# Kernel optimization log

Measured on AMD Instinct MI355X. Metric: run time of the kernel, lower is better.

Reference implementation:

```python
import jax, jax.numpy as jnp
import numpy as np

B, S, DM = 4, 4096, 1024
H, DH = 16, 64          # num_attention_heads, attention_head_size
K = 128                 # Linformer projection dim (k_dims)


def setup_inputs() -> dict:
    key = jax.random.key(0)
    ks = jax.random.split(key, 9)
    s = 1.0 / np.sqrt(DM)
    return {
        "hidden_states": jax.random.normal(ks[0], (B, S, DM), jnp.float32),
        "Wq": jax.random.normal(ks[1], (DM, DM), jnp.float32) * s,
        "bq": jax.random.normal(ks[2], (DM,), jnp.float32) * 0.02,
        "Wk": jax.random.normal(ks[3], (DM, DM), jnp.float32) * s,
        "bk": jax.random.normal(ks[4], (DM,), jnp.float32) * 0.02,
        "Wv": jax.random.normal(ks[5], (DM, DM), jnp.float32) * s,
        "bv": jax.random.normal(ks[6], (DM,), jnp.float32) * 0.02,
        # E, D: [k_dims, max_input_len], init randn/sqrt(k_dims) as in torch module
        "E": jax.random.normal(ks[7], (K, S), jnp.float32) / np.sqrt(K),
        "D": jax.random.normal(ks[8], (K, S), jnp.float32) / np.sqrt(K),
    }


def reference(hidden_states, Wq, bq, Wk, bk, Wv, bv, E, D):
    b, s, _ = hidden_states.shape

    def heads(x):  # [b,s,DM] -> [b,H,s,DH]
        return x.reshape(b, s, H, DH).transpose(0, 2, 1, 3)

    # torch Linear: y = x @ W.T + b
    q = heads(hidden_states @ Wq.T + bq)   # [b,H,s,DH]
    k = heads(hidden_states @ Wk.T + bk)   # [b,H,s,DH]
    v = heads(hidden_states @ Wv.T + bv)   # [b,H,s,DH]

    # Linformer low-rank projection along the sequence axis
    pk = jnp.einsum('ks,bhsd->bhkd', E[:, :s], k)  # [b,H,K,DH]
    pv = jnp.einsum('ks,bhsd->bhkd', D[:, :s], v)  # [b,H,K,DH]

    scores = jnp.einsum('bhsd,bhkd->bhsk', q, pk) / np.sqrt(DH).astype(np.float32)
    probs = jax.nn.softmax(scores, axis=-1)        # [b,H,s,K]
    ctx = jnp.einsum('bhsk,bhkd->bhsd', probs, pv) # [b,H,s,DH]
    return ctx.transpose(0, 2, 1, 3).reshape(b, s, H * DH)
```

## Files before the change

### kernel.cpp

```cpp
#include <hip/hip_runtime.h>
#include <hip/hip_bf16.h>
#include <stdint.h>


typedef __attribute__((ext_vector_type(8))) _Float16 f16x8;
typedef __attribute__((ext_vector_type(4))) _Float16 f16x4;
typedef __attribute__((ext_vector_type(4))) float    f32x4;

__device__ __forceinline__ f32x4 mfma16(f16x8 a, f16x8 b, f32x4 c) {
    return __builtin_amdgcn_mfma_f32_16x16x32_f16(a, b, c, 0, 0, 0);
}

__device__ __forceinline__ void gload16(const void* g, void* l) {
    __builtin_amdgcn_global_load_lds(
        (const __attribute__((address_space(1))) void*)g,
        (__attribute__((address_space(3))) void*)l, 16, 0, 0);
}

__global__ __launch_bounds__(256) void cvt_f16(const float* __restrict__ in,
                                               _Float16* __restrict__ out, int n4) {
    int i = blockIdx.x * 256 + threadIdx.x;
    int stride = gridDim.x * 256;
    for (; i < n4; i += stride) {
        f32x4 v = reinterpret_cast<const f32x4*>(in)[i];
        f16x4 o;
#pragma unroll
        for (int j = 0; j < 4; ++j) o[j] = (_Float16)v[j];
        reinterpret_cast<f16x4*>(out)[i] = o;
    }
}

__global__ __launch_bounds__(256) void cvt_f16_2(const float* __restrict__ in0,
                                                 _Float16* __restrict__ out0,
                                                 const float* __restrict__ in1,
                                                 _Float16* __restrict__ out1, int n4) {
    const float* in = blockIdx.y ? in1 : in0;
    _Float16* out = blockIdx.y ? out1 : out0;
    int i = blockIdx.x * 256 + threadIdx.x;
    int stride = gridDim.x * 256;
    for (; i < n4; i += stride) {
        f32x4 v = reinterpret_cast<const f32x4*>(in)[i];
        f16x4 o;
#pragma unroll
        for (int j = 0; j < 4; ++j) o[j] = (_Float16)v[j];
        reinterpret_cast<f16x4*>(out)[i] = o;
    }
}

__global__ __launch_bounds__(256) void cvt_hilo2(const float* __restrict__ in0,
                                                 _Float16* __restrict__ hi0,
                                                 _Float16* __restrict__ lo0,
                                                 const float* __restrict__ in1,
                                                 _Float16* __restrict__ hi1,
                                                 _Float16* __restrict__ lo1, int n4) {
    const float* in = blockIdx.y ? in1 : in0;
    _Float16* hi = blockIdx.y ? hi1 : hi0;
    _Float16* lo = blockIdx.y ? lo1 : lo0;
    int i = blockIdx.x * 256 + threadIdx.x;
    int stride = gridDim.x * 256;
    for (; i < n4; i += stride) {
        f32x4 v = reinterpret_cast<const f32x4*>(in)[i];
        f16x4 h, l;
#pragma unroll
        for (int j = 0; j < 4; ++j) {
            _Float16 hb = (_Float16)v[j];
            h[j] = hb;
            l[j] = (_Float16)(v[j] - (float)hb);
        }
        reinterpret_cast<f16x4*>(hi)[i] = h;
        reinterpret_cast<f16x4*>(lo)[i] = l;
    }
}

__global__ __launch_bounds__(256) void rowsum_k(const float* __restrict__ E,
                                                const float* __restrict__ D,
                                                float* __restrict__ sE,
                                                float* __restrict__ sD) {
    __shared__ float red[256];
    const int blk = blockIdx.x;
    const float* src = (blk < 128) ? E : D;
    float* dst = (blk < 128) ? sE : sD;
    const int row = blk & 127;
    float s = 0.f;
    for (int i = threadIdx.x; i < 4096; i += 256) s += src[(size_t)row * 4096 + i];
    red[threadIdx.x] = s;
    __syncthreads();
    for (int off = 128; off > 0; off >>= 1) {
        if ((int)threadIdx.x < off) red[threadIdx.x] += red[threadIdx.x + off];
        __syncthreads();
    }
    if (threadIdx.x == 0) dst[row] = red[0];
}

__global__ __launch_bounds__(256) void gemm_q_f16(
    const _Float16* __restrict__ A, const _Float16* __restrict__ B,
    const float* __restrict__ bias, _Float16* __restrict__ Q) {
    const int Kd = 1024, N = 1024, NT = 16;
    __shared__ _Float16 Asm[2][128 * 64];
    __shared__ _Float16 Bsm[2][128 * 64];
    const int tid = threadIdx.x, lane = tid & 63, wave = tid >> 6;
    const int l15 = lane & 15, lg = lane >> 4;
    const int row0 = blockIdx.x * 128, col0 = blockIdx.y * 128;
    const int wr = (wave >> 1) * 64, wc = (wave & 1) * 64;
    f32x4 acc[4][4];
#pragma unroll
    for (int m = 0; m < 4; ++m)
#pragma unroll
        for (int n = 0; n < 4; ++n) acc[m][n] = (f32x4)0.0f;

    const _Float16* aSrc[4];
    const _Float16* bSrc[4];
    int ub[4];
#pragma unroll
    for (int it = 0; it < 4; ++it) {
        int u = it * 256 + tid;
        int r = u >> 3, c = u & 7;
        int sc = (c ^ (r & 7)) * 8;
        aSrc[it] = A + (size_t)(row0 + r) * Kd + sc;
        bSrc[it] = B + (size_t)(col0 + r) * Kd + sc;
        ub[it] = it * 256 + wave * 64;
    }
    auto stage = [&](int buf, int t) {
        const int k0 = t * 64;
#pragma unroll
        for (int it = 0; it < 4; ++it) {
            gload16(aSrc[it] + k0, &Asm[buf][ub[it] * 8]);
            gload16(bSrc[it] + k0, &Bsm[buf][ub[it] * 8]);
        }
    };

    stage(0, 0);
#pragma unroll 1
    for (int t = 0; t < NT; ++t) {
        const int cur = t & 1;
        if (t < NT - 1) {
            stage(cur ^ 1, t + 1);
            asm volatile("s_waitcnt vmcnt(8)" ::: "memory");
        } else {
            asm volatile("s_waitcnt vmcnt(0)" ::: "memory");
        }
        __builtin_amdgcn_s_barrier();
#pragma unroll
        for (int kk = 0; kk < 2; ++kk) {
            f16x8 af[4], bfr[4];
#pragma unroll
            for (int m = 0; m < 4; ++m)
                af[m] = *reinterpret_cast<const f16x8*>(
                    &Asm[cur][(wr + m * 16 + l15) * 64 + (((kk * 4 + lg) ^ (l15 & 7)) * 8)]);
#pragma unroll
            for (int n = 0; n < 4; ++n)
                bfr[n] = *reinterpret_cast<const f16x8*>(
                    &Bsm[cur][(wc + n * 16 + l15) * 64 + (((kk * 4 + lg) ^ (l15 & 7)) * 8)]);
#pragma unroll
            for (int m = 0; m < 4; ++m)
#pragma unroll
                for (int n = 0; n < 4; ++n) acc[m][n] = mfma16(af[m], bfr[n], acc[m][n]);
        }
        __builtin_amdgcn_s_barrier();
    }
#pragma unroll
    for (int m = 0; m < 4; ++m)
#pragma unroll
        for (int n = 0; n < 4; ++n) {
            int colg = col0 + wc + n * 16 + l15;
            float bi = bias[colg];
#pragma unroll
            for (int r = 0; r < 4; ++r) {
                int rowg = row0 + wr + m * 16 + lg * 4 + r;
                Q[(size_t)rowg * N + colg] = (_Float16)(acc[m][n][r] + bi);
            }
        }
}

__global__ __launch_bounds__(256) void eproj2(const _Float16* __restrict__ EB,
                                              const _Float16* __restrict__ DB,
                                              const _Float16* __restrict__ X,
                                              float* __restrict__ EHf,
                                              float* __restrict__ DHf) {
    __shared__ _Float16 Ea[128 * 72];
    __shared__ _Float16 BT[128 * 72];
    const int tid = threadIdx.x, lane = tid & 63, wave = tid >> 6;
    const int l15 = lane & 15, lg = lane >> 4;
    const int sc = blockIdx.x;
    const int n0 = blockIdx.y * 128;
    const int bb = blockIdx.z & 3;
    const _Float16* Emat = (blockIdx.z >> 2) ? DB : EB;
    float* Of = (blockIdx.z >> 2) ? DHf : EHf;
    const int wr = (wave >> 1) * 64, wc = (wave & 1) * 64;
    const int nb = tid & 31, sb = tid >> 5;
    f32x4 acc[4][4];
#pragma unroll
    for (int m = 0; m < 4; ++m)
#pragma unroll
        for (int n = 0; n < 4; ++n) acc[m][n] = (f32x4)0.0f;

    for (int ks = 0; ks < 512; ks += 64) {
        const int s0 = sc * 512 + ks;
        __syncthreads();
#pragma unroll
        for (int i = 0; i < 4; ++i) {
            int u = tid + 256 * i;
            int r = u >> 3, c8 = (u & 7) * 8;
            *reinterpret_cast<f16x8*>(&Ea[r * 72 + c8]) =
                *reinterpret_cast<const f16x8*>(Emat + (size_t)r * 4096 + s0 + c8);
        }
        {
            f16x4 rr[8];
#pragma unroll
            for (int i = 0; i < 8; ++i)
                rr[i] = *reinterpret_cast<const f16x4*>(
                    X + (size_t)(bb * 4096 + s0 + sb * 8 + i) * 1024 + n0 + nb * 4);
#pragma unroll
            for (int j = 0; j < 4; ++j) {
                f16x8 w;
#pragma unroll
                for (int i = 0; i < 8; ++i) w[i] = rr[i][j];
                *reinterpret_cast<f16x8*>(&BT[(nb * 4 + j) * 72 + sb * 8]) = w;
            }
        }
        __syncthreads();
#pragma unroll
        for (int kk = 0; kk < 2; ++kk) {
            f16x8 af[4], bfr[4];
#pragma unroll
            for (int m = 0; m < 4; ++m)
                af[m] = *reinterpret_cast<const f16x8*>(
                    &Ea[(wr + m * 16 + l15) * 72 + kk * 32 + lg * 8]);
#pragma unroll
            for (int n = 0; n < 4; ++n)
                bfr[n] = *reinterpret_cast<const f16x8*>(
                    &BT[(wc + n * 16 + l15) * 72 + kk * 32 + lg * 8]);
#pragma unroll
            for (int m = 0; m < 4; ++m)
#pragma unroll
                for (int n = 0; n < 4; ++n) acc[m][n] = mfma16(af[m], bfr[n], acc[m][n]);
        }
    }
#pragma unroll
    for (int m = 0; m < 4; ++m)
#pragma unroll
        for (int n = 0; n < 4; ++n)
#pragma unroll
            for (int r = 0; r < 4; ++r)
                atomicAdd(&Of[(size_t)(bb * 128 + wr + m * 16 + lg * 4 + r) * 1024 +
                              n0 + wc + n * 16 + l15],
                          acc[m][n][r]);
}

__global__ __launch_bounds__(256) void gemm_split2(
    const float* __restrict__ A0, const _Float16* __restrict__ Bh0,
    const _Float16* __restrict__ Bl0, const float* __restrict__ bias0,
    const float* __restrict__ rs0, _Float16* __restrict__ PKH,
    const float* __restrict__ A1, const _Float16* __restrict__ Bh1,
    const _Float16* __restrict__ Bl1, const float* __restrict__ bias1,
    const float* __restrict__ rs1, _Float16* __restrict__ PVT) {
    const int Kd = 1024;
    const float* A = blockIdx.z ? A1 : A0;
    const _Float16* Bh = blockIdx.z ? Bh1 : Bh0;
    const _Float16* Bl = blockIdx.z ? Bl1 : Bl0;
    const float* bias = blockIdx.z ? bias1 : bias0;
    const float* rowscale = blockIdx.z ? rs1 : rs0;
    __shared__ _Float16 Ah[64 * 40], Al[64 * 40], Bhs[64 * 40], Bls[64 * 40];
    const int tid = threadIdx.x, lane = tid & 63, wave = tid >> 6;
    const int l15 = lane & 15, lg = lane >> 4;
    const int row0 = blockIdx.x * 64, col0 = blockIdx.y * 64;
    const int wr = (wave >> 1) * 32, wc = (wave & 1) * 32;
    f32x4 acc[2][2];
#pragma unroll
    for (int m = 0; m < 2; ++m)
#pragma unroll
        for (int n = 0; n < 2; ++n) acc[m][n] = (f32x4)0.0f;

    const int r = tid >> 2, c8 = (tid & 3) * 8;
    for (int k0 = 0; k0 < Kd; k0 += 32) {
        __syncthreads();
        {
            const float* src = A + (size_t)(row0 + r) * Kd + k0 + c8;
            f32x4 v0 = *reinterpret_cast<const f32x4*>(src);
            f32x4 v1 = *reinterpret_cast<const f32x4*>(src + 4);
            f16x8 h8, l8;
#pragma unroll
            for (int j = 0; j < 4; ++j) {
                _Float16 hb = (_Float16)v0[j];
                h8[j] = hb; l8[j] = (_Float16)(v0[j] - (float)hb);
            }
#pragma unroll
            for (int j = 0; j < 4; ++j) {
                _Float16 hb = (_Float16)v1[j];
                h8[4 + j] = hb; l8[4 + j] = (_Float16)(v1[j] - (float)hb);
            }
            *reinterpret_cast<f16x8*>(&Ah[r * 40 + c8]) = h8;
            *reinterpret_cast<f16x8*>(&Al[r * 40 + c8]) = l8;
            *reinterpret_cast<f16x8*>(&Bhs[r * 40 + c8]) =
                *reinterpret_cast<const f16x8*>(Bh + (size_t)(col0 + r) * Kd + k0 + c8);
            *reinterpret_cast<f16x8*>(&Bls[r * 40 + c8]) =
                *reinterpret_cast<const f16x8*>(Bl + (size_t)(col0 + r) * Kd + k0 + c8);
        }
        __syncthreads();
        f16x8 ah[2], al[2], bh[2], bl[2];
#pragma unroll
        for (int m = 0; m < 2; ++m) {
            ah[m] = *reinterpret_cast<const f16x8*>(&Ah[(wr + m * 16 + l15) * 40 + lg * 8]);
            al[m] = *reinterpret_cast<const f16x8*>(&Al[(wr + m * 16 + l15) * 40 + lg * 8]);
        }
#pragma unroll
        for (int n = 0; n < 2; ++n) {
            bh[n] = *reinterpret_cast<const f16x8*>(&Bhs[(wc + n * 16 + l15) * 40 + lg * 8]);
            bl[n] = *reinterpret_cast<const f16x8*>(&Bls[(wc + n * 16 + l15) * 40 + lg * 8]);
        }
#pragma unroll
        for (int m = 0; m < 2; ++m)
#pragma unroll
            for (int n = 0; n < 2; ++n) {
                acc[m][n] = mfma16(ah[m], bh[n], acc[m][n]);
                acc[m][n] = mfma16(al[m], bh[n], acc[m][n]);
                acc[m][n] = mfma16(ah[m], bl[n], acc[m][n]);
            }
    }
#pragma unroll
    for (int m = 0; m < 2; ++m)
#pragma unroll
        for (int n = 0; n < 2; ++n) {
            int colg = col0 + wc + n * 16 + l15;
            float bi = bias[colg];
#pragma unroll
            for (int rr2 = 0; rr2 < 4; ++rr2) {
                int rowg = row0 + wr + m * 16 + lg * 4 + rr2;
                float val = acc[m][n][rr2] + rowscale[rowg & 127] * bi;
                if (blockIdx.z == 0) {
                    PKH[(size_t)rowg * 1024 + colg] = (_Float16)(val * 0.125f);
                } else {
                    PVT[(size_t)((rowg >> 7) * 16 + (colg >> 6)) * 8192 +
                        (colg & 63) * 128 + (rowg & 127)] = (_Float16)val;
                }
            }
        }
}

__global__ __launch_bounds__(256, 4) void attn_fused(
    const _Float16* __restrict__ QH, const _Float16* __restrict__ PKH,
    const _Float16* __restrict__ PVT, float* __restrict__ Out) {
    __shared__ _Float16 smem[16384];
    const int tid = threadIdx.x, lane = tid & 63, wave = tid >> 6;
    const int l15 = lane & 15, lg = lane >> 4;
    const int st = blockIdx.x, h = blockIdx.y, bb = blockIdx.z;

    {
        const _Float16* pkh_g = PKH + (size_t)(bb * 128) * 1024 + h * 64;
        const _Float16* pvt_g = PVT + (size_t)(bb * 16 + h) * 8192;
        const int su = wave * 64 + lane;
#pragma unroll
        for (int it = 0; it < 4; ++it) {
            int u = it * 256 + su;
            int ub = it * 256 + wave * 64;
            {
                int r = u >> 3, c = u & 7;
                int sc = (c ^ (r & 7)) * 8;
                gload16(pkh_g + (size_t)r * 1024 + sc, &smem[ub * 8]);
            }
            {
                int r = u >> 4, c = u & 15;
                int sc = (c ^ (r & 7)) * 8;
                gload16(pvt_g + r * 128 + sc, &smem[8192 + ub * 8]);
            }
        }
    }
    const int srow0 = bb * 4096 + st * 128 + wave * 32;
    f16x8 qf[2][2];
#pragma unroll
    for (int m = 0; m < 2; ++m)
#pragma unroll
        for (int kk = 0; kk < 2; ++kk)
            qf[m][kk] = *reinterpret_cast<const f16x8*>(
                QH + (size_t)(srow0 + m * 16 + l15) * 1024 + h * 64 + kk * 32 + lg * 8);
    __syncthreads();

    f32x4 accT[8][2];
#pragma unroll
    for (int n = 0; n < 8; ++n)
#pragma unroll
        for (int m = 0; m < 2; ++m) accT[n][m] = (f32x4)0.0f;
#pragma unroll
    for (int kk = 0; kk < 2; ++kk)
#pragma unroll
        for (int n = 0; n < 8; ++n) {
            f16x8 pk = *reinterpret_cast<const f16x8*>(
                &smem[(n * 16 + l15) * 64 + (((kk * 4 + lg) ^ (l15 & 7)) * 8)]);
#pragma unroll
            for (int m = 0; m < 2; ++m)
                accT[n][m] = mfma16(pk, qf[m][kk], accT[n][m]);
        }
    __syncthreads();

#pragma unroll
    for (int m = 0; m < 2; ++m) {
        float v = -1e30f;
#pragma unroll
        for (int n = 0; n < 8; ++n)
#pragma unroll
            for (int r = 0; r < 4; ++r) v = fmaxf(v, accT[n][m][r]);
        v = fmaxf(v, __shfl_xor(v, 16));
        v = fmaxf(v, __shfl_xor(v, 32));
        float s = 0.f;
#pragma unroll
        for (int n = 0; n < 8; ++n)
#pragma unroll
            for (int r = 0; r < 4; ++r) {
                float e = __expf(accT[n][m][r] - v);
                accT[n][m][r] = e;
                s += e;
            }
        s += __shfl_xor(s, 16);
        s += __shfl_xor(s, 32);
        float inv = 1.0f / s;
#pragma unroll
        for (int n = 0; n < 8; ++n)
#pragma unroll
            for (int r = 0; r < 4; ++r) accT[n][m][r] *= inv;
    }

    _Float16* pw = smem + wave * 2048;
    f32x4 o[2][4];
#pragma unroll
    for (int m = 0; m < 2; ++m)
#pragma unroll
        for (int n = 0; n < 4; ++n) o[m][n] = (f32x4)0.0f;
#pragma unroll
    for (int half = 0; half < 2; ++half) {
#pragma unroll
        for (int nl = 0; nl < 4; ++nl) {
            int n = half * 4 + nl;
#pragma unroll
            for (int m = 0; m < 2; ++m) {
                int q = l15 + 16 * m;
                int kp = (nl * 8 + lg * 2) ^ ((q & 7) << 2);
                f16x4 v;
#pragma unroll
                for (int r = 0; r < 4; ++r) v[r] = (_Float16)accT[n][m][r];
                *reinterpret_cast<f16x4*>(&pw[q * 64 + kp * 2]) = v;
            }
        }
#pragma unroll
        for (int ksl = 0; ksl < 2; ++ksl) {
            f16x8 pa[2];
#pragma unroll
            for (int m = 0; m < 2; ++m) {
                int q = m * 16 + l15;
                int kpb = (ksl * 16 + lg * 4) ^ ((q & 7) << 2);
                pa[m] = *reinterpret_cast<const f16x8*>(&pw[q * 64 + kpb * 2]);
            }
            int ks = half * 2 + ksl;
#pragma unroll
            for (int n = 0; n < 4; ++n) {
                int dd = n * 16 + l15;
                f16x8 bv = *reinterpret_cast<const f16x8*>(
                    &smem[8192 + dd * 128 + (((ks * 4 + lg) ^ (dd & 7)) * 8)]);
#pragma unroll
                for (int m = 0; m < 2; ++m) o[m][n] = mfma16(pa[m], bv, o[m][n]);
            }
        }
    }

#pragma unroll
    for (int m = 0; m < 2; ++m)
#pragma unroll
        for (int n = 0; n < 4; ++n)
#pragma unroll
            for (int r = 0; r < 4; ++r) {
                int row = srow0 + m * 16 + lg * 4 + r;
                Out[(size_t)row * 1024 + h * 64 + n * 16 + l15] = o[m][n][r];
            }
}

extern "C" void kernel_launch(void* const* d_in, const int* in_sizes, int n_in,
                              void* d_out, int out_size, void* d_ws, size_t ws_size,
                              hipStream_t stream) {
    const float* hs = (const float*)d_in[0];
    const float* Wq = (const float*)d_in[1];
    const float* bq = (const float*)d_in[2];
    const float* Wk = (const float*)d_in[3];
    const float* bk = (const float*)d_in[4];
    const float* Wv = (const float*)d_in[5];
    const float* bv = (const float*)d_in[6];
    const float* Em = (const float*)d_in[7];
    const float* Dm = (const float*)d_in[8];
    float* out = (float*)d_out;
    char* ws = (char*)d_ws;

    _Float16* hsB = (_Float16*)(ws + 0);
    _Float16* WqB = (_Float16*)(ws + 33554432);
    _Float16* WkH = (_Float16*)(ws + 35651584);
    _Float16* WkL = (_Float16*)(ws + 37748736);
    _Float16* WvH = (_Float16*)(ws + 39845888);
    _Float16* WvL = (_Float16*)(ws + 41943040);
    _Float16* EB  = (_Float16*)(ws + 44040192);
    _Float16* DB  = (_Float16*)(ws + 45088768);
    float* sE  = (float*)(ws + 46137344);
    float* sD  = (float*)(ws + 46137856);
    _Float16* QHq = (_Float16*)(ws + 46138368);
    float* EHf = (float*)(ws + 113247232);
    float* DHf = (float*)(ws + 115344384);
    _Float16* PKH = (_Float16*)(ws + 117441536);
    _Float16* PVT = (_Float16*)(ws + 118490112);

    cvt_f16<<<2048, 256, 0, stream>>>(hs, hsB, 16777216 / 4);
    cvt_f16<<<1024, 256, 0, stream>>>(Wq, WqB, 1048576 / 4);
    cvt_hilo2<<<dim3(1024, 2), 256, 0, stream>>>(Wk, WkH, WkL, Wv, WvH, WvL,
                                                 1048576 / 4);
    cvt_f16_2<<<dim3(512, 2), 256, 0, stream>>>(Em, EB, Dm, DB, 524288 / 4);
    rowsum_k<<<256, 256, 0, stream>>>(Em, Dm, sE, sD);
    gemm_q_f16<<<dim3(128, 8), 256, 0, stream>>>(hsB, WqB, bq, QHq);
    hipMemsetAsync(EHf, 0, 2 * 512 * 1024 * sizeof(float), stream);
    eproj2<<<dim3(8, 8, 8), 256, 0, stream>>>(EB, DB, hsB, EHf, DHf);
    gemm_split2<<<dim3(8, 16, 2), 256, 0, stream>>>(EHf, WkH, WkL, bk, sE, PKH,
                                                    DHf, WvH, WvL, bv, sD, PVT);
    attn_fused<<<dim3(32, 16, 4), 256, 0, stream>>>(QHq, PKH, PVT, out);
}
```

Measured before the change: 166.0 us.

## Fuse prep kernels, single-buffer Q GEMM with occupancy hint, halve eproj split

Merges the five conversion and rowsum kernels into one launch that dispatches work by block index, cutting launch overhead. The Q-projection GEMM drops LDS double buffering in favour of one synchronous buffer, with a launch-bounds hint of 4 blocks per CU to raise occupancy. The E/D sequence projection now gives each block 1024 sequence positions instead of 512, halving the grid and the atomic/partial accumulation. The Q GEMM gives up copy/compute overlap within a block in exchange for more resident blocks, and eproj runs on fewer blocks.

```diff
diff --git a/kernel.cpp b/kernel.cpp
--- a/kernel.cpp
+++ b/kernel.cpp
@@ -17,87 +17,88 @@
         (__attribute__((address_space(3))) void*)l, 16, 0, 0);
 }
 
-__global__ __launch_bounds__(256) void cvt_f16(const float* __restrict__ in,
-                                               _Float16* __restrict__ out, int n4) {
-    int i = blockIdx.x * 256 + threadIdx.x;
-    int stride = gridDim.x * 256;
-    for (; i < n4; i += stride) {
-        f32x4 v = reinterpret_cast<const f32x4*>(in)[i];
-        f16x4 o;
-#pragma unroll
-        for (int j = 0; j < 4; ++j) o[j] = (_Float16)v[j];
-        reinterpret_cast<f16x4*>(out)[i] = o;
-    }
-}
-
-__global__ __launch_bounds__(256) void cvt_f16_2(const float* __restrict__ in0,
-                                                 _Float16* __restrict__ out0,
-                                                 const float* __restrict__ in1,
-                                                 _Float16* __restrict__ out1, int n4) {
-    const float* in = blockIdx.y ? in1 : in0;
-    _Float16* out = blockIdx.y ? out1 : out0;
-    int i = blockIdx.x * 256 + threadIdx.x;
-    int stride = gridDim.x * 256;
-    for (; i < n4; i += stride) {
-        f32x4 v = reinterpret_cast<const f32x4*>(in)[i];
-        f16x4 o;
-#pragma unroll
-        for (int j = 0; j < 4; ++j) o[j] = (_Float16)v[j];
-        reinterpret_cast<f16x4*>(out)[i] = o;
-    }
-}
-
-__global__ __launch_bounds__(256) void cvt_hilo2(const float* __restrict__ in0,
-                                                 _Float16* __restrict__ hi0,
-                                                 _Float16* __restrict__ lo0,
-                                                 const float* __restrict__ in1,
-                                                 _Float16* __restrict__ hi1,
-                                                 _Float16* __restrict__ lo1, int n4) {
-    const float* in = blockIdx.y ? in1 : in0;
-    _Float16* hi = blockIdx.y ? hi1 : hi0;
-    _Float16* lo = blockIdx.y ? lo1 : lo0;
-    int i = blockIdx.x * 256 + threadIdx.x;
-    int stride = gridDim.x * 256;
-    for (; i < n4; i += stride) {
-        f32x4 v = reinterpret_cast<const f32x4*>(in)[i];
-        f16x4 h, l;
-#pragma unroll
-        for (int j = 0; j < 4; ++j) {
-            _Float16 hb = (_Float16)v[j];
-            h[j] = hb;
-            l[j] = (_Float16)(v[j] - (float)hb);
-        }
-        reinterpret_cast<f16x4*>(hi)[i] = h;
-        reinterpret_cast<f16x4*>(lo)[i] = l;
-    }
-}
-
-__global__ __launch_bounds__(256) void rowsum_k(const float* __restrict__ E,
-                                                const float* __restrict__ D,
-                                                float* __restrict__ sE,
-                                                float* __restrict__ sD) {
+__global__ __launch_bounds__(256) void prep_all(
+    const float* __restrict__ hs, _Float16* __restrict__ hsB,
+    const float* __restrict__ Wq, _Float16* __restrict__ WqB,
+    const float* __restrict__ Wk, _Float16* __restrict__ WkH, _Float16* __restrict__ WkL,
+    const float* __restrict__ Wv, _Float16* __restrict__ WvH, _Float16* __restrict__ WvL,
+    const float* __restrict__ Em, _Float16* __restrict__ EB,
+    const float* __restrict__ Dm, _Float16* __restrict__ DB,
+    float* __restrict__ sE, float* __restrict__ sD) {
     __shared__ float red[256];
-    const int blk = blockIdx.x;
-    const float* src = (blk < 128) ? E : D;
-    float* dst = (blk < 128) ? sE : sD;
-    const int row = blk & 127;
-    float s = 0.f;
-    for (int i = threadIdx.x; i < 4096; i += 256) s += src[(size_t)row * 4096 + i];
-    red[threadIdx.x] = s;
-    __syncthreads();
-    for (int off = 128; off > 0; off >>= 1) {
-        if ((int)threadIdx.x < off) red[threadIdx.x] += red[threadIdx.x + off];
-        __syncthreads();
-    }
-    if (threadIdx.x == 0) dst[row] = red[0];
-}
-
-__global__ __launch_bounds__(256) void gemm_q_f16(
+    const int blk = blockIdx.x, tid = threadIdx.x;
+
+    if (blk < 2048) {
+        int i = blk * 256 + tid;
+        for (; i < 4194304; i += 2048 * 256) {
+            f32x4 v = reinterpret_cast<const f32x4*>(hs)[i];
+            f16x4 o;
+#pragma unroll
+            for (int j = 0; j < 4; ++j) o[j] = (_Float16)v[j];
+            reinterpret_cast<f16x4*>(hsB)[i] = o;
+        }
+    } else if (blk < 2304) {
+        int i = (blk - 2048) * 256 + tid;
+        for (; i < 262144; i += 256 * 256) {
+            f32x4 v = reinterpret_cast<const f32x4*>(Wq)[i];
+            f16x4 o;
+#pragma unroll
+            for (int j = 0; j < 4; ++j) o[j] = (_Float16)v[j];
+            reinterpret_cast<f16x4*>(WqB)[i] = o;
+        }
+    } else if (blk < 2816) {
+        const int sect = (blk - 2304) >> 8;
+        const float* in = sect ? Wv : Wk;
+        _Float16* hi = sect ? WvH : WkH;
+        _Float16* lo = sect ? WvL : WkL;
+        int i = ((blk - 2304) & 255) * 256 + tid;
+        for (; i < 262144; i += 256 * 256) {
+            f32x4 v = reinterpret_cast<const f32x4*>(in)[i];
+            f16x4 h, l;
+#pragma unroll
+            for (int j = 0; j < 4; ++j) {
+                _Float16 hb = (_Float16)v[j];
+                h[j] = hb;
+                l[j] = (_Float16)(v[j] - (float)hb);
+            }
+            reinterpret_cast<f16x4*>(hi)[i] = h;
+            reinterpret_cast<f16x4*>(lo)[i] = l;
+        }
+    } else if (blk < 3072) {
+        const int sect = (blk - 2816) >> 7;
+        const float* in = sect ? Dm : Em;
+        _Float16* out = sect ? DB : EB;
+        int i = ((blk - 2816) & 127) * 256 + tid;
+        for (; i < 131072; i += 128 * 256) {
+            f32x4 v = reinterpret_cast<const f32x4*>(in)[i];
+            f16x4 o;
+#pragma unroll
+            for (int j = 0; j < 4; ++j) o[j] = (_Float16)v[j];
+            reinterpret_cast<f16x4*>(out)[i] = o;
+        }
+    } else {
+        const int rb = blk - 3072;
+        const float* src = (rb < 128) ? Em : Dm;
+        float* dst = (rb < 128) ? sE : sD;
+        const int row = rb & 127;
+        float s = 0.f;
+        for (int i = tid; i < 4096; i += 256) s += src[(size_t)row * 4096 + i];
+        red[tid] = s;
+        __syncthreads();
+        for (int off = 128; off > 0; off >>= 1) {
+            if (tid < off) red[tid] += red[tid + off];
+            __syncthreads();
+        }
+        if (tid == 0) dst[row] = red[0];
+    }
+}
+
+__global__ __launch_bounds__(256, 4) void gemm_q_f16(
     const _Float16* __restrict__ A, const _Float16* __restrict__ B,
     const float* __restrict__ bias, _Float16* __restrict__ Q) {
     const int Kd = 1024, N = 1024, NT = 16;
-    __shared__ _Float16 Asm[2][128 * 64];
-    __shared__ _Float16 Bsm[2][128 * 64];
+    __shared__ _Float16 Asm[128 * 64];
+    __shared__ _Float16 Bsm[128 * 64];
     const int tid = threadIdx.x, lane = tid & 63, wave = tid >> 6;
     const int l15 = lane & 15, lg = lane >> 4;
     const int row0 = blockIdx.x * 128, col0 = blockIdx.y * 128;
@@ -120,43 +121,36 @@
         bSrc[it] = B + (size_t)(col0 + r) * Kd + sc;
         ub[it] = it * 256 + wave * 64;
     }
-    auto stage = [&](int buf, int t) {
-        const int k0 = t * 64;
-#pragma unroll
-        for (int it = 0; it < 4; ++it) {
-            gload16(aSrc[it] + k0, &Asm[buf][ub[it] * 8]);
-            gload16(bSrc[it] + k0, &Bsm[buf][ub[it] * 8]);
-        }
-    };
-
-    stage(0, 0);
+
 #pragma unroll 1
     for (int t = 0; t < NT; ++t) {
-        const int cur = t & 1;
-        if (t < NT - 1) {
-            stage(cur ^ 1, t + 1);
-            asm volatile("s_waitcnt vmcnt(8)" ::: "memory");
-        } else {
-            asm volatile("s_waitcnt vmcnt(0)" ::: "memory");
-        }
-        __builtin_amdgcn_s_barrier();
+        __syncthreads();
+        const int k0 = t * 64;
+#pragma unroll
+        for (int it = 0; it < 4; ++it)
+            gload16(aSrc[it] + k0, &Asm[ub[it] * 8]);
+#pragma unroll
+        for (int it = 0; it < 4; ++it)
+            gload16(bSrc[it] + k0, &Bsm[ub[it] * 8]);
+        asm volatile("s_waitcnt vmcnt(0)" ::: "memory");
+        __syncthreads();
 #pragma unroll
         for (int kk = 0; kk < 2; ++kk) {
+            const int ksw = ((kk * 4 + lg) ^ (l15 & 7)) * 8;
             f16x8 af[4], bfr[4];
 #pragma unroll
             for (int m = 0; m < 4; ++m)
                 af[m] = *reinterpret_cast<const f16x8*>(
-                    &Asm[cur][(wr + m * 16 + l15) * 64 + (((kk * 4 + lg) ^ (l15 & 7)) * 8)]);
+                    &Asm[(wr + m * 16 + l15) * 64 + ksw]);
 #pragma unroll
             for (int n = 0; n < 4; ++n)
                 bfr[n] = *reinterpret_cast<const f16x8*>(
-                    &Bsm[cur][(wc + n * 16 + l15) * 64 + (((kk * 4 + lg) ^ (l15 & 7)) * 8)]);
+                    &Bsm[(wc + n * 16 + l15) * 64 + ksw]);
 #pragma unroll
             for (int m = 0; m < 4; ++m)
 #pragma unroll
                 for (int n = 0; n < 4; ++n) acc[m][n] = mfma16(af[m], bfr[n], acc[m][n]);
         }
-        __builtin_amdgcn_s_barrier();
     }
 #pragma unroll
     for (int m = 0; m < 4; ++m)
@@ -194,8 +188,8 @@
 #pragma unroll
         for (int n = 0; n < 4; ++n) acc[m][n] = (f32x4)0.0f;
 
-    for (int ks = 0; ks < 512; ks += 64) {
-        const int s0 = sc * 512 + ks;
+    for (int ks = 0; ks < 1024; ks += 64) {
+        const int s0 = sc * 1024 + ks;
         __syncthreads();
 #pragma unroll
         for (int i = 0; i < 4; ++i) {
@@ -503,15 +497,11 @@
     _Float16* PKH = (_Float16*)(ws + 117441536);
     _Float16* PVT = (_Float16*)(ws + 118490112);
 
-    cvt_f16<<<2048, 256, 0, stream>>>(hs, hsB, 16777216 / 4);
-    cvt_f16<<<1024, 256, 0, stream>>>(Wq, WqB, 1048576 / 4);
-    cvt_hilo2<<<dim3(1024, 2), 256, 0, stream>>>(Wk, WkH, WkL, Wv, WvH, WvL,
-                                                 1048576 / 4);
-    cvt_f16_2<<<dim3(512, 2), 256, 0, stream>>>(Em, EB, Dm, DB, 524288 / 4);
-    rowsum_k<<<256, 256, 0, stream>>>(Em, Dm, sE, sD);
+    prep_all<<<3328, 256, 0, stream>>>(hs, hsB, Wq, WqB, Wk, WkH, WkL,
+                                       Wv, WvH, WvL, Em, EB, Dm, DB, sE, sD);
     gemm_q_f16<<<dim3(128, 8), 256, 0, stream>>>(hsB, WqB, bq, QHq);
     hipMemsetAsync(EHf, 0, 2 * 512 * 1024 * sizeof(float), stream);
-    eproj2<<<dim3(8, 8, 8), 256, 0, stream>>>(EB, DB, hsB, EHf, DHf);
+    eproj2<<<dim3(4, 8, 8), 256, 0, stream>>>(EB, DB, hsB, EHf, DHf);
     gemm_split2<<<dim3(8, 16, 2), 256, 0, stream>>>(EHf, WkH, WkL, bk, sE, PKH,
                                                     DHf, WvH, WvL, bv, sD, PVT);
     attn_fused<<<dim3(32, 16, 4), 256, 0, stream>>>(QHq, PKH, PVT, out);
```

New measurement: 151.8 us. 1.09x faster.
